# Optimization experiments

Measured on AMD Instinct MI355X. Metric: run time of the kernel, lower is better.

## Reference

```python
import jax, jax.numpy as jnp
import numpy as np

U_N = 100000
I_N = 50000
EMB_DIM = 64
L_N = 3          # number of propagation layers
NNZ = 4_800_000  # edges in the normalized bipartite graph (avg degree ~32)


def setup_inputs() -> dict:
    key = jax.random.key(0)
    k_u, k_i, k_r, k_c, k_v = jax.random.split(key, 5)
    N = U_N + I_N
    # Xavier-uniform-ish embedding init
    lim = float(np.sqrt(6.0 / (U_N + EMB_DIM)))
    user_emb = jax.random.uniform(k_u, (U_N, EMB_DIM), jnp.float32, -lim, lim)
    lim_i = float(np.sqrt(6.0 / (I_N + EMB_DIM)))
    item_emb = jax.random.uniform(k_i, (I_N, EMB_DIM), jnp.float32, -lim_i, lim_i)
    # COO sparse graph over all N = u_n + i_n nodes
    row = jax.random.randint(k_r, (NNZ,), 0, N, jnp.int32)
    col = jax.random.randint(k_c, (NNZ,), 0, N, jnp.int32)
    # emulate symmetric-normalized adjacency values ~ 1/deg so propagation stays bounded
    vals = jax.random.uniform(k_v, (NNZ,), jnp.float32) * (1.0 / 32.0)
    return {"user_emb": user_emb, "item_emb": item_emb, "row": row, "col": col, "vals": vals}


def reference(user_emb, item_emb, row, col, vals):
    N = user_emb.shape[0] + item_emb.shape[0]
    all_emb = jnp.concatenate([user_emb, item_emb], axis=0)  # [N, D]
    emb0 = all_emb
    acc = all_emb  # running sum over layer embeddings (layer 0 included)
    x = all_emb
    for _ in range(L_N):
        # SpMM: out[r] += vals[e] * x[col[e]] for each edge e with row[e] == r
        x = jax.ops.segment_sum(vals[:, None] * x[col], row, num_segments=N)
        acc = acc + x
    out = acc / (L_N + 1)  # mean over stacked layer embeddings
    return (emb0, out)
```

## Files before the change

kernel.cpp:

```cpp
#include <hip/hip_runtime.h>

#define U_N 100000
#define I_N 50000
#define N_NODES 150000
#define EMB_D 64
#define NNZ 4800000
#define ND (N_NODES * EMB_D)
#define ND4 (ND / 4)
#define UD4 (U_N * EMB_D / 4)

#define RPB 256
#define NB ((N_NODES + RPB - 1) / RPB)
#define TILE 2048
#define NTILE ((NNZ + TILE - 1) / TILE)
#define HTILE 4096
#define NHT ((NNZ + HTILE - 1) / HTILE)

__device__ __forceinline__ unsigned short f2bf(float f) {
    unsigned int u = __float_as_uint(f);
    unsigned int r = (u + 0x7FFFu + ((u >> 16) & 1u)) >> 16;
    return (unsigned short)r;
}
__device__ __forceinline__ float bf2f(unsigned short h) {
    return __uint_as_float((unsigned int)h << 16);
}

__global__ void k_init(const float4* __restrict__ u, const float4* __restrict__ it,
                       float4* __restrict__ emb0, ushort4* __restrict__ hb0) {
    int i = blockIdx.x * blockDim.x + threadIdx.x;
    if (i >= ND4) return;
    float4 v = (i < UD4) ? u[i] : it[i - UD4];
    emb0[i] = v;
    ushort4 h;
    h.x = f2bf(v.x); h.y = f2bf(v.y); h.z = f2bf(v.z); h.w = f2bf(v.w);
    hb0[i] = h;
}

__global__ void k_bucket_hist(const int4* __restrict__ row4, int* __restrict__ bhist) {
    __shared__ int lh[NB];
    int t = threadIdx.x;
    for (int i = t; i < NB; i += 256) lh[i] = 0;
    __syncthreads();
    int base = blockIdx.x * (HTILE / 4);
    int cnt = min(HTILE / 4, NNZ / 4 - base);
    for (int i = t; i < cnt; i += 256) {
        int4 r = row4[base + i];
        atomicAdd(&lh[r.x >> 8], 1);
        atomicAdd(&lh[r.y >> 8], 1);
        atomicAdd(&lh[r.z >> 8], 1);
        atomicAdd(&lh[r.w >> 8], 1);
    }
    __syncthreads();
    for (int i = t; i < NB; i += 256)
        if (lh[i]) atomicAdd(&bhist[i], lh[i]);
}

__global__ void k_bucket_scan(const int* __restrict__ bhist, int* __restrict__ bbase,
                              int* __restrict__ bcur) {
    __shared__ int wsum[16];
    int t = threadIdx.x, lane = t & 63, wv = t >> 6;
    int v = (t < NB) ? bhist[t] : 0;
    int iv = v;
    for (int off = 1; off < 64; off <<= 1) {
        int u = __shfl_up(iv, off);
        if (lane >= off) iv += u;
    }
    if (lane == 63) wsum[wv] = iv;
    __syncthreads();
    int woff = 0;
    for (int w = 0; w < wv; ++w) woff += wsum[w];
    int ex = woff + iv - v;
    if (t < NB) { bbase[t] = ex; bcur[t] = ex; }
    if (t == NB - 1) bbase[NB] = ex + v;
}

__global__ void k_partition(const int* __restrict__ row, const int* __restrict__ col,
                            const float* __restrict__ vals, int* __restrict__ bcur,
                            int2* __restrict__ tmp) {
    __shared__ int2 stage[TILE];
    __shared__ unsigned short stageB[TILE];
    __shared__ int hist[NB];
    __shared__ int scn[NB];
    __shared__ int gbase[NB];
    __shared__ int wsum[4];
    int t = threadIdx.x;
    int lane = t & 63, wv = t >> 6;
    for (int i = t; i < NB; i += 256) hist[i] = 0;
    __syncthreads();
    int base = blockIdx.x * TILE;
    int cnt = min(TILE, NNZ - base);

    int  myb[8];
    int  myslot[8];
    int2 myp[8];
#pragma unroll
    for (int j = 0; j < 8; ++j) {
        int i = t + j * 256;
        myb[j] = -1;
        if (i < cnt) {
            int e = base + i;
            int r = row[e];
            int b = r >> 8;
            myb[j] = b;
            myp[j] = make_int2(((r & (RPB - 1)) << 18) | col[e], __float_as_int(vals[e]));
            myslot[j] = atomicAdd(&hist[b], 1);
        }
    }
    __syncthreads();
    int carry = 0;
    for (int c0 = 0; c0 < NB; c0 += 256) {
        int idx = c0 + t;
        int v = (idx < NB) ? hist[idx] : 0;
        int iv = v;
        for (int off = 1; off < 64; off <<= 1) {
            int u = __shfl_up(iv, off);
            if (lane >= off) iv += u;
        }
        if (lane == 63) wsum[wv] = iv;
        __syncthreads();
        int woff = 0;
        for (int w = 0; w < wv; ++w) woff += wsum[w];
        if (idx < NB) scn[idx] = carry + woff + iv - v;
        carry += wsum[0] + wsum[1] + wsum[2] + wsum[3];
        __syncthreads();
    }
    for (int idx = t; idx < NB; idx += 256) {
        int h = hist[idx];
        if (h > 0) gbase[idx] = atomicAdd(&bcur[idx], h);
    }
    __syncthreads();
#pragma unroll
    for (int j = 0; j < 8; ++j) {
        if (myb[j] >= 0) {
            int pos = scn[myb[j]] + myslot[j];
            stage[pos] = myp[j];
            stageB[pos] = (unsigned short)myb[j];
        }
    }
    __syncthreads();
    for (int i = t; i < cnt; i += 256) {
        int b = stageB[i];
        tmp[gbase[b] + (i - scn[b])] = stage[i];
    }
}

__global__ void k_bucket_csr(const int* __restrict__ bbase, const int2* __restrict__ tmp,
                             int2* __restrict__ edges, int* __restrict__ rp) {
    __shared__ int lh[RPB];
    __shared__ int lex[RPB];
    __shared__ int wsum[4];
    int b = blockIdx.x, t = threadIdx.x;
    int lane = t & 63, wv = t >> 6;
    int s0 = bbase[b], s1 = bbase[b + 1];
    int n = s1 - s0;
    lh[t] = 0;
    __syncthreads();
    for (int i = t; i < n; i += 256)
        atomicAdd(&lh[(unsigned)tmp[s0 + i].x >> 18], 1);
    __syncthreads();
    int v = lh[t];
    int iv = v;
    for (int off = 1; off < 64; off <<= 1) {
        int u = __shfl_up(iv, off);
        if (lane >= off) iv += u;
    }
    if (lane == 63) wsum[wv] = iv;
    __syncthreads();
    int woff = 0;
    for (int w = 0; w < wv; ++w) woff += wsum[w];
    int excl = woff + iv - v;
    int r = b * RPB + t;
    if (r < N_NODES) rp[r] = s0 + excl;
    if (b == NB - 1 && t == 0) rp[N_NODES] = NNZ;
    lex[t] = excl;
    __syncthreads();
    for (int i = t; i < n; i += 256) {
        int2 p = tmp[s0 + i];
        int rl = (unsigned)p.x >> 18;
        int pos = s0 + atomicAdd(&lex[rl], 1);
        edges[pos] = make_int2(p.x & 0x3FFFF, p.y);
    }
}

__device__ __forceinline__ float row_dot(const int* __restrict__ rp,
                                         const int2* __restrict__ edges,
                                         const unsigned short* __restrict__ x,
                                         int wid, int lane) {
    int start = __builtin_amdgcn_readfirstlane(rp[wid]);
    int end   = __builtin_amdgcn_readfirstlane(rp[wid + 1]);
    float s0 = 0.f, s1 = 0.f, s2 = 0.f, s3 = 0.f;
    int e = start;
    for (; e + 16 <= end; e += 16) {
        int2 E[16];
#pragma unroll
        for (int j = 0; j < 16; ++j) E[j] = edges[e + j];
        float g[16];
#pragma unroll
        for (int j = 0; j < 16; ++j) g[j] = bf2f(x[(size_t)E[j].x * EMB_D + lane]);
#pragma unroll
        for (int j = 0; j < 16; ++j) {
            float p = __int_as_float(E[j].y) * g[j];
            if ((j & 3) == 0) s0 += p;
            else if ((j & 3) == 1) s1 += p;
            else if ((j & 3) == 2) s2 += p;
            else s3 += p;
        }
    }
    int rem = end - e;
    if (rem > 0) {
        int2 E[16];
#pragma unroll
        for (int j = 0; j < 16; ++j) E[j] = edges[e + j];
#pragma unroll
        for (int j = 0; j < 16; ++j)
            if (j >= rem) { E[j].x = 0; E[j].y = 0; }
        float g[16];
#pragma unroll
        for (int j = 0; j < 16; ++j) g[j] = bf2f(x[(size_t)E[j].x * EMB_D + lane]);
#pragma unroll
        for (int j = 0; j < 16; ++j) {
            float p = __int_as_float(E[j].y) * g[j];
            if ((j & 3) == 0) s0 += p;
            else if ((j & 3) == 1) s1 += p;
            else if ((j & 3) == 2) s2 += p;
            else s3 += p;
        }
    }
    return (s0 + s1) + (s2 + s3);
}

__global__ void k_spmm_mid(const int* __restrict__ rp, const int2* __restrict__ edges,
                           const unsigned short* __restrict__ x,
                           unsigned short* __restrict__ y) {
    int wid = blockIdx.x * (blockDim.x >> 6) + (threadIdx.x >> 6);
    if (wid >= N_NODES) return;
    int lane = threadIdx.x & 63;
    float s = row_dot(rp, edges, x, wid, lane);
    y[(size_t)wid * EMB_D + lane] = f2bf(s);
}

__global__ void k_spmm_fin(const int* __restrict__ rp, const int2* __restrict__ edges,
                           const unsigned short* __restrict__ x,
                           const float* __restrict__ emb0,
                           const unsigned short* __restrict__ y1,
                           const unsigned short* __restrict__ y2,
                           float* __restrict__ acc) {
    int wid = blockIdx.x * (blockDim.x >> 6) + (threadIdx.x >> 6);
    if (wid >= N_NODES) return;
    int lane = threadIdx.x & 63;
    float s = row_dot(rp, edges, x, wid, lane);
    size_t o = (size_t)wid * EMB_D + lane;
    acc[o] = (emb0[o] + bf2f(y1[o]) + bf2f(y2[o]) + s) * 0.25f;
}

extern "C" void kernel_launch(void* const* d_in, const int* in_sizes, int n_in,
                              void* d_out, int out_size, void* d_ws, size_t ws_size,
                              hipStream_t stream) {
    const float* user_emb = (const float*)d_in[0];
    const float* item_emb = (const float*)d_in[1];
    const int*   row      = (const int*)d_in[2];
    const int*   col      = (const int*)d_in[3];
    const float* vals     = (const float*)d_in[4];

    float* emb0 = (float*)d_out;
    float* acc  = (float*)d_out + ND;

    int2* tmp   = (int2*)d_ws;
    int2* edges = tmp + NNZ;
    unsigned short* hb2 = (unsigned short*)(edges + NNZ);
    int*  ibase = (int*)(hb2 + ND);
    int*  rp    = ibase;
    int*  bhist = ibase + N_NODES + 1;
    int*  bbase = bhist + NB;
    int*  bcur  = bbase + NB + 1;
    unsigned short* hb0 = (unsigned short*)d_ws;
    unsigned short* hb1 = hb0 + ND;

    const int BLK = 256;
    const int grid_nd = (ND4 + BLK - 1) / BLK;
    const int grid_spmm = (N_NODES * 64 + BLK - 1) / BLK;

    hipMemsetAsync(bhist, 0, NB * sizeof(int), stream);
    k_bucket_hist<<<NHT, BLK, 0, stream>>>((const int4*)row, bhist);
    k_bucket_scan<<<1, 1024, 0, stream>>>(bhist, bbase, bcur);
    k_partition<<<NTILE, BLK, 0, stream>>>(row, col, vals, bcur, tmp);
    k_bucket_csr<<<NB, BLK, 0, stream>>>(bbase, tmp, edges, rp);

    k_init<<<grid_nd, BLK, 0, stream>>>((const float4*)user_emb,
                                        (const float4*)item_emb,
                                        (float4*)emb0, (ushort4*)hb0);

    k_spmm_mid<<<grid_spmm, BLK, 0, stream>>>(rp, edges, hb0, hb1);
    k_spmm_mid<<<grid_spmm, BLK, 0, stream>>>(rp, edges, hb1, hb2);
    k_spmm_fin<<<grid_spmm, BLK, 0, stream>>>(rp, edges, hb2, emb0, hb1, hb2, acc);
}
```

Baseline: 615.1 us.

## Coarsen CSR build buckets to 1024 rows with per-wave privatized histograms

Row buckets grow from 256 to 1024 rows, which cuts the bucket count to 147. The partition tile doubles to 4096 edges and runs on 512 threads, and its multi-pass block scan becomes a single pass over per-wave histograms with cumulative wave offsets. The histogram and CSR kernels use per-wave or per-group privatized shared histograms to reduce LDS atomic contention, and the CSR kernel runs 1024 threads per bucket. The goal is cheaper graph preprocessing, at the cost of more shared memory per block and larger per-bucket work in the CSR stage.

```diff
diff --git a/kernel.cpp b/kernel.cpp
--- a/kernel.cpp
+++ b/kernel.cpp
@@ -9,9 +9,9 @@
 #define ND4 (ND / 4)
 #define UD4 (U_N * EMB_D / 4)
 
-#define RPB 256
+#define RPB 1024
 #define NB ((N_NODES + RPB - 1) / RPB)
-#define TILE 2048
+#define TILE 4096
 #define NTILE ((NNZ + TILE - 1) / TILE)
 #define HTILE 4096
 #define NHT ((NNZ + HTILE - 1) / HTILE)
@@ -37,27 +37,29 @@
 }
 
 __global__ void k_bucket_hist(const int4* __restrict__ row4, int* __restrict__ bhist) {
-    __shared__ int lh[NB];
-    int t = threadIdx.x;
-    for (int i = t; i < NB; i += 256) lh[i] = 0;
+    __shared__ int lh[4][NB];
+    int t = threadIdx.x, wv = t >> 6;
+    for (int i = t; i < 4 * NB; i += 256) ((int*)lh)[i] = 0;
     __syncthreads();
     int base = blockIdx.x * (HTILE / 4);
     int cnt = min(HTILE / 4, NNZ / 4 - base);
     for (int i = t; i < cnt; i += 256) {
         int4 r = row4[base + i];
-        atomicAdd(&lh[r.x >> 8], 1);
-        atomicAdd(&lh[r.y >> 8], 1);
-        atomicAdd(&lh[r.z >> 8], 1);
-        atomicAdd(&lh[r.w >> 8], 1);
-    }
-    __syncthreads();
-    for (int i = t; i < NB; i += 256)
-        if (lh[i]) atomicAdd(&bhist[i], lh[i]);
+        atomicAdd(&lh[wv][r.x >> 10], 1);
+        atomicAdd(&lh[wv][r.y >> 10], 1);
+        atomicAdd(&lh[wv][r.z >> 10], 1);
+        atomicAdd(&lh[wv][r.w >> 10], 1);
+    }
+    __syncthreads();
+    for (int i = t; i < NB; i += 256) {
+        int s = lh[0][i] + lh[1][i] + lh[2][i] + lh[3][i];
+        if (s) atomicAdd(&bhist[i], s);
+    }
 }
 
 __global__ void k_bucket_scan(const int* __restrict__ bhist, int* __restrict__ bbase,
                               int* __restrict__ bcur) {
-    __shared__ int wsum[16];
+    __shared__ int wsum[4];
     int t = threadIdx.x, lane = t & 63, wv = t >> 6;
     int v = (t < NB) ? bhist[t] : 0;
     int iv = v;
@@ -78,14 +80,15 @@
                             const float* __restrict__ vals, int* __restrict__ bcur,
                             int2* __restrict__ tmp) {
     __shared__ int2 stage[TILE];
-    __shared__ unsigned short stageB[TILE];
-    __shared__ int hist[NB];
+    __shared__ unsigned char stageB[TILE];
+    __shared__ int whist[8][NB];
+    __shared__ int cumw[8][NB];
     __shared__ int scn[NB];
     __shared__ int gbase[NB];
-    __shared__ int wsum[4];
+    __shared__ int wsum[8];
     int t = threadIdx.x;
     int lane = t & 63, wv = t >> 6;
-    for (int i = t; i < NB; i += 256) hist[i] = 0;
+    for (int i = t; i < 8 * NB; i += 512) ((int*)whist)[i] = 0;
     __syncthreads();
     int base = blockIdx.x * TILE;
     int cnt = min(TILE, NNZ - base);
@@ -95,50 +98,51 @@
     int2 myp[8];
 #pragma unroll
     for (int j = 0; j < 8; ++j) {
-        int i = t + j * 256;
+        int i = t + j * 512;
         myb[j] = -1;
         if (i < cnt) {
             int e = base + i;
             int r = row[e];
-            int b = r >> 8;
+            int b = r >> 10;
             myb[j] = b;
             myp[j] = make_int2(((r & (RPB - 1)) << 18) | col[e], __float_as_int(vals[e]));
-            myslot[j] = atomicAdd(&hist[b], 1);
-        }
-    }
-    __syncthreads();
-    int carry = 0;
-    for (int c0 = 0; c0 < NB; c0 += 256) {
-        int idx = c0 + t;
-        int v = (idx < NB) ? hist[idx] : 0;
-        int iv = v;
-        for (int off = 1; off < 64; off <<= 1) {
-            int u = __shfl_up(iv, off);
-            if (lane >= off) iv += u;
-        }
-        if (lane == 63) wsum[wv] = iv;
-        __syncthreads();
-        int woff = 0;
-        for (int w = 0; w < wv; ++w) woff += wsum[w];
-        if (idx < NB) scn[idx] = carry + woff + iv - v;
-        carry += wsum[0] + wsum[1] + wsum[2] + wsum[3];
-        __syncthreads();
-    }
-    for (int idx = t; idx < NB; idx += 256) {
-        int h = hist[idx];
-        if (h > 0) gbase[idx] = atomicAdd(&bcur[idx], h);
-    }
+            myslot[j] = atomicAdd(&whist[wv][b], 1);
+        }
+    }
+    __syncthreads();
+    int v = 0;
+    if (t < NB) {
+        int run = 0;
+#pragma unroll
+        for (int w = 0; w < 8; ++w) {
+            cumw[w][t] = run;
+            run += whist[w][t];
+        }
+        v = run;
+    }
+    int iv = v;
+    for (int off = 1; off < 64; off <<= 1) {
+        int u = __shfl_up(iv, off);
+        if (lane >= off) iv += u;
+    }
+    if (lane == 63) wsum[wv] = iv;
+    __syncthreads();
+    int woff = 0;
+    for (int w = 0; w < wv; ++w) woff += wsum[w];
+    if (t < NB) scn[t] = woff + iv - v;
+    if (t < NB && v > 0) gbase[t] = atomicAdd(&bcur[t], v);
     __syncthreads();
 #pragma unroll
     for (int j = 0; j < 8; ++j) {
         if (myb[j] >= 0) {
-            int pos = scn[myb[j]] + myslot[j];
+            int b = myb[j];
+            int pos = scn[b] + cumw[wv][b] + myslot[j];
             stage[pos] = myp[j];
-            stageB[pos] = (unsigned short)myb[j];
-        }
-    }
-    __syncthreads();
-    for (int i = t; i < cnt; i += 256) {
+            stageB[pos] = (unsigned char)b;
+        }
+    }
+    __syncthreads();
+    for (int i = t; i < cnt; i += 512) {
         int b = stageB[i];
         tmp[gbase[b] + (i - scn[b])] = stage[i];
     }
@@ -146,19 +150,20 @@
 
 __global__ void k_bucket_csr(const int* __restrict__ bbase, const int2* __restrict__ tmp,
                              int2* __restrict__ edges, int* __restrict__ rp) {
-    __shared__ int lh[RPB];
+    __shared__ int ph[4][RPB];
     __shared__ int lex[RPB];
-    __shared__ int wsum[4];
+    __shared__ int wsum[16];
     int b = blockIdx.x, t = threadIdx.x;
     int lane = t & 63, wv = t >> 6;
     int s0 = bbase[b], s1 = bbase[b + 1];
     int n = s1 - s0;
-    lh[t] = 0;
-    __syncthreads();
-    for (int i = t; i < n; i += 256)
-        atomicAdd(&lh[(unsigned)tmp[s0 + i].x >> 18], 1);
-    __syncthreads();
-    int v = lh[t];
+    for (int i = t; i < 4 * RPB; i += 1024) ((int*)ph)[i] = 0;
+    __syncthreads();
+    int cp = wv >> 2;
+    for (int i = t; i < n; i += 1024)
+        atomicAdd(&ph[cp][(unsigned)tmp[s0 + i].x >> 18], 1);
+    __syncthreads();
+    int v = ph[0][t] + ph[1][t] + ph[2][t] + ph[3][t];
     int iv = v;
     for (int off = 1; off < 64; off <<= 1) {
         int u = __shfl_up(iv, off);
@@ -172,12 +177,12 @@
     int r = b * RPB + t;
     if (r < N_NODES) rp[r] = s0 + excl;
     if (b == NB - 1 && t == 0) rp[N_NODES] = NNZ;
-    lex[t] = excl;
-    __syncthreads();
-    for (int i = t; i < n; i += 256) {
+    lex[t] = s0 + excl;
+    __syncthreads();
+    for (int i = t; i < n; i += 1024) {
         int2 p = tmp[s0 + i];
         int rl = (unsigned)p.x >> 18;
-        int pos = s0 + atomicAdd(&lex[rl], 1);
+        int pos = atomicAdd(&lex[rl], 1);
         edges[pos] = make_int2(p.x & 0x3FFFF, p.y);
     }
 }
@@ -282,9 +287,9 @@
 
     hipMemsetAsync(bhist, 0, NB * sizeof(int), stream);
     k_bucket_hist<<<NHT, BLK, 0, stream>>>((const int4*)row, bhist);
-    k_bucket_scan<<<1, 1024, 0, stream>>>(bhist, bbase, bcur);
-    k_partition<<<NTILE, BLK, 0, stream>>>(row, col, vals, bcur, tmp);
-    k_bucket_csr<<<NB, BLK, 0, stream>>>(bbase, tmp, edges, rp);
+    k_bucket_scan<<<1, BLK, 0, stream>>>(bhist, bbase, bcur);
+    k_partition<<<NTILE, 512, 0, stream>>>(row, col, vals, bcur, tmp);
+    k_bucket_csr<<<NB, 1024, 0, stream>>>(bbase, tmp, edges, rp);
 
     k_init<<<grid_nd, BLK, 0, stream>>>((const float4*)user_emb,
                                         (const float4*)item_emb,
```

Result: faster. 570.7 us, median of 2 (-7.2%).
